# Performance work log

Measured on AMD Instinct MI355X. Metric: run time of the kernel, lower is better.

Reference implementation:

```python
import jax, jax.numpy as jnp
import numpy as np

N = 50000
DIM = 64
E = 800000


def setup_inputs() -> dict:
    key = jax.random.key(0)
    ks = jax.random.split(key, 12)
    s = 1.0 / np.sqrt(DIM)
    inp = {
        "x": jax.random.normal(ks[0], (N, DIM), dtype=jnp.float32),
        "coord": jax.random.normal(ks[1], (N, DIM), dtype=jnp.float32),
        "Wq": jax.random.uniform(ks[2], (DIM, DIM), jnp.float32, -s, s),
        "bq": jax.random.uniform(ks[3], (DIM,), jnp.float32, -s, s),
        "Wk": jax.random.uniform(ks[4], (DIM, DIM), jnp.float32, -s, s),
        "bk": jax.random.uniform(ks[5], (DIM,), jnp.float32, -s, s),
        "Wv": jax.random.uniform(ks[6], (DIM, DIM), jnp.float32, -s, s),
        "bv": jax.random.uniform(ks[7], (DIM,), jnp.float32, -s, s),
        "Wc": jax.random.uniform(ks[8], (DIM, 1), jnp.float32, -1.0, 1.0),
        "bc": jax.random.uniform(ks[9], (DIM,), jnp.float32, -1.0, 1.0),
        "edge_index": jax.random.randint(ks[10], (2, E), 0, N, dtype=jnp.int64),
    }
    return inp


def reference(x, coord, Wq, bq, Wk, bk, Wv, bv, Wc, bc, edge_index):
    row, col = edge_index[0], edge_index[1]
    # per-edge coordinate differences and distances: [E, DIM], [E, 1]
    dx = coord[row] - coord[col]
    dist = jnp.linalg.norm(dx, axis=-1, keepdims=True)
    # per-edge QKV projections (torch Linear: x @ W.T + b): [E, DIM]
    q = x[row] @ Wq.T + bq
    k = x[col] @ Wk.T + bk
    v = x[col] @ Wv.T + bv
    # scalar attention logit per edge, GLOBAL softmax over all edges (dim=0)
    attn = jnp.sum(q * k, axis=-1, keepdims=True)  # [E, 1]
    weight = jax.nn.softmax(attn, axis=0)          # [E, 1]
    delta_x = weight * v                            # [E, DIM]
    delta_coord = weight * (dist @ Wc.T + bc) * dx  # [E, DIM]
    # scatter-add back to nodes
    x_out = jax.ops.segment_sum(delta_x, row, num_segments=x.shape[0])
    coord_out = jax.ops.segment_sum(delta_coord, row, num_segments=coord.shape[0])
    return (x + x_out, coord + coord_out)
```

## Files before the change

### kernel.cpp

```cpp
#include <hip/hip_runtime.h>
#include <math.h>

#define N_NODES 50000
#define DIM 64
#define NE 800000
#define NSCAN_BLOCKS ((N_NODES + 255) / 256)

static __device__ __forceinline__ float bf2f(unsigned short u) {
    return __uint_as_float(((unsigned int)u) << 16);
}
static __device__ __forceinline__ unsigned short f2bf(float f) {
    unsigned int u = __float_as_uint(f);
    u += 0x7fffu + ((u >> 16) & 1u);
    return (unsigned short)(u >> 16);
}


__global__ __launch_bounds__(256, 5) void k_qkv(
    const float* __restrict__ x, const float* __restrict__ coord,
    const float* __restrict__ Wq, const float* __restrict__ bq,
    const float* __restrict__ Wk, const float* __restrict__ bk,
    const float* __restrict__ Wv, const float* __restrict__ bv,
    float* __restrict__ Qf, unsigned short* __restrict__ Kb,
    unsigned short* __restrict__ Vb, unsigned short* __restrict__ Cb)
{
    __shared__ ushort4 WT2[3][1024];
    __shared__ float4  xs4[32][16];

    const int tid  = threadIdx.x;
    const int base = blockIdx.x * 32;

    for (int t = tid; t < 1024; t += 256) {
        int d = t & 63, j2 = t >> 6;
        float4 a = ((const float4*)Wq)[d * 16 + j2];
        float4 b = ((const float4*)Wk)[d * 16 + j2];
        float4 c = ((const float4*)Wv)[d * 16 + j2];
        WT2[0][t] = make_ushort4(f2bf(a.x), f2bf(a.y), f2bf(a.z), f2bf(a.w));
        WT2[1][t] = make_ushort4(f2bf(b.x), f2bf(b.y), f2bf(b.z), f2bf(b.w));
        WT2[2][t] = make_ushort4(f2bf(c.x), f2bf(c.y), f2bf(c.z), f2bf(c.w));
    }
    for (int t = tid; t < 32 * DIM; t += 256) {
        if (base + (t >> 6) < N_NODES)
            Cb[(size_t)base * DIM + t] = f2bf(coord[(size_t)base * DIM + t]);
    }
    for (int t = tid; t < 512; t += 256) {
        int r = t >> 4, j2 = t & 15;
        if (base + r < N_NODES)
            xs4[r][j2] = ((const float4*)x)[(size_t)(base + r) * 16 + j2];
    }
    __syncthreads();

    const int wv = tid >> 6;
    const int d  = tid & 63;
    const float bqv = bq[d], bkv = bk[d], bvv = bv[d];

    float aq[8], ak[8], av[8];
    #pragma unroll
    for (int r = 0; r < 8; ++r) { aq[r] = bqv; ak[r] = bkv; av[r] = bvv; }

    #pragma unroll 4
    for (int j2 = 0; j2 < 16; ++j2) {
        ushort4 uq = WT2[0][j2 * 64 + d];
        ushort4 uk = WT2[1][j2 * 64 + d];
        ushort4 uv = WT2[2][j2 * 64 + d];
        float wqx = bf2f(uq.x), wqy = bf2f(uq.y), wqz = bf2f(uq.z), wqw = bf2f(uq.w);
        float wkx = bf2f(uk.x), wky = bf2f(uk.y), wkz = bf2f(uk.z), wkw = bf2f(uk.w);
        float wvx = bf2f(uv.x), wvy = bf2f(uv.y), wvz = bf2f(uv.z), wvw = bf2f(uv.w);
        #pragma unroll
        for (int r = 0; r < 8; ++r) {
            float4 xv = xs4[wv * 8 + r][j2];
            aq[r] += xv.x * wqx + xv.y * wqy + xv.z * wqz + xv.w * wqw;
            ak[r] += xv.x * wkx + xv.y * wky + xv.z * wkz + xv.w * wkw;
            av[r] += xv.x * wvx + xv.y * wvy + xv.z * wvz + xv.w * wvw;
        }
    }
    #pragma unroll
    for (int r = 0; r < 8; ++r) {
        int n = base + wv * 8 + r;
        if (n < N_NODES) {
            Qf[(size_t)n * DIM + d] = aq[r];
            Kb[(size_t)n * DIM + d] = f2bf(ak[r]);
            Vb[(size_t)n * DIM + d] = f2bf(av[r]);
        }
    }
}

__global__ __launch_bounds__(256) void k_hist(
    const int* __restrict__ eidx, int* __restrict__ counts)
{
    int e = blockIdx.x * 256 + threadIdx.x;
    if (e < NE) atomicAdd(counts + eidx[e], 1);
}

__global__ __launch_bounds__(256) void k_scan1(
    const int* __restrict__ counts, int* __restrict__ offsets,
    int* __restrict__ bsums)
{
    __shared__ int tmp[256];
    int i = blockIdx.x * 256 + threadIdx.x;
    int v = (i < N_NODES) ? counts[i] : 0;
    tmp[threadIdx.x] = v;
    __syncthreads();
    #pragma unroll
    for (int off = 1; off < 256; off <<= 1) {
        int t = (threadIdx.x >= off) ? tmp[threadIdx.x - off] : 0;
        __syncthreads();
        tmp[threadIdx.x] += t;
        __syncthreads();
    }
    if (i < N_NODES) offsets[i] = tmp[threadIdx.x] - v;
    if (threadIdx.x == 255) bsums[blockIdx.x] = tmp[255];
}

__global__ __launch_bounds__(256) void k_scan2(int* __restrict__ bsums)
{
    __shared__ int tmp[256];
    int i = threadIdx.x;
    int v = (i < NSCAN_BLOCKS) ? bsums[i] : 0;
    tmp[i] = v;
    __syncthreads();
    #pragma unroll
    for (int off = 1; off < 256; off <<= 1) {
        int t = (i >= off) ? tmp[i - off] : 0;
        __syncthreads();
        tmp[i] += t;
        __syncthreads();
    }
    if (i < NSCAN_BLOCKS) bsums[i] = tmp[i] - v;
}

__global__ __launch_bounds__(256) void k_scan3(
    int* __restrict__ offsets, int* __restrict__ counts,
    const int* __restrict__ bsums)
{
    int i = blockIdx.x * 256 + threadIdx.x;
    if (i < N_NODES) {
        int o = offsets[i] + bsums[i >> 8];
        offsets[i] = o;
        counts[i]  = o;
    }
    if (i == 0) offsets[N_NODES] = NE;
}

__global__ __launch_bounds__(256) void k_fill(
    const int* __restrict__ eidx, int* __restrict__ cursor,
    int* __restrict__ bucket_col)
{
    int e = blockIdx.x * 256 + threadIdx.x;
    if (e < NE) {
        int pos = atomicAdd(cursor + eidx[e], 1);
        bucket_col[pos] = eidx[NE + e];
    }
}

__global__ __launch_bounds__(256) void k_edge_fused(
    const int* __restrict__ bucket_col, const int* __restrict__ offsets,
    const float* __restrict__ Qf, const unsigned short* __restrict__ Kb,
    const unsigned short* __restrict__ Vb, const unsigned short* __restrict__ Cb,
    const float* __restrict__ coord,
    const float* __restrict__ Wc, const float* __restrict__ bc,
    float* __restrict__ out_x, float* __restrict__ out_c,
    float* __restrict__ wsum)
{
    const int lane = threadIdx.x & 63;
    const int n = (blockIdx.x * 256 + threadIdx.x) >> 6;
    if (n >= N_NODES) return;
    const int qt = lane >> 4;
    const int sl = lane & 15;

    const float4 q4  = ((const float4*)Qf)[(size_t)n * 16 + sl];
    const float4 cr4 = ((const float4*)coord)[(size_t)n * 16 + sl];
    const float4 wc4 = ((const float4*)Wc)[sl];
    const float4 bc4 = ((const float4*)bc)[sl];

    const int s = offsets[n], t = offsets[n + 1];
    float4 accx = {0.f, 0.f, 0.f, 0.f};
    float4 accc = {0.f, 0.f, 0.f, 0.f};
    float psum = 0.0f;

    for (int base = s; base < t; base += 8) {
        int pos0 = base + qt;
        int pos1 = base + 4 + qt;
        bool valid0 = pos0 < t, valid1 = pos1 < t;
        int pc0 = valid0 ? pos0 : (t - 1);
        int pc1 = valid1 ? pos1 : (t - 1);
        int c0 = bucket_col[pc0];
        int c1 = bucket_col[pc1];
        size_t rb0 = (size_t)c0 * 16 + sl;
        size_t rb1 = (size_t)c1 * 16 + sl;
        ushort4 ku0 = ((const ushort4*)Kb)[rb0];
        ushort4 vu0 = ((const ushort4*)Vb)[rb0];
        ushort4 cu0 = ((const ushort4*)Cb)[rb0];
        ushort4 ku1 = ((const ushort4*)Kb)[rb1];
        ushort4 vu1 = ((const ushort4*)Vb)[rb1];
        ushort4 cu1 = ((const ushort4*)Cb)[rb1];

        float d0 = q4.x * bf2f(ku0.x) + q4.y * bf2f(ku0.y)
                 + q4.z * bf2f(ku0.z) + q4.w * bf2f(ku0.w);
        float dx0x = cr4.x - bf2f(cu0.x), dx0y = cr4.y - bf2f(cu0.y);
        float dx0z = cr4.z - bf2f(cu0.z), dx0w = cr4.w - bf2f(cu0.w);
        float e0 = dx0x * dx0x + dx0y * dx0y + dx0z * dx0z + dx0w * dx0w;
        float d1 = q4.x * bf2f(ku1.x) + q4.y * bf2f(ku1.y)
                 + q4.z * bf2f(ku1.z) + q4.w * bf2f(ku1.w);
        float dx1x = cr4.x - bf2f(cu1.x), dx1y = cr4.y - bf2f(cu1.y);
        float dx1z = cr4.z - bf2f(cu1.z), dx1w = cr4.w - bf2f(cu1.w);
        float e1 = dx1x * dx1x + dx1y * dx1y + dx1z * dx1z + dx1w * dx1w;

        #pragma unroll
        for (int off = 1; off <= 8; off <<= 1) {
            d0 += __shfl_xor(d0, off);
            e0 += __shfl_xor(e0, off);
            d1 += __shfl_xor(d1, off);
            e1 += __shfl_xor(e1, off);
        }
        float p0 = valid0 ? __expf(d0) : 0.0f;
        float p1 = valid1 ? __expf(d1) : 0.0f;
        float dist0 = sqrtf(e0), dist1 = sqrtf(e1);
        psum += p0 + p1;
        accx.x += p0 * bf2f(vu0.x) + p1 * bf2f(vu1.x);
        accx.y += p0 * bf2f(vu0.y) + p1 * bf2f(vu1.y);
        accx.z += p0 * bf2f(vu0.z) + p1 * bf2f(vu1.z);
        accx.w += p0 * bf2f(vu0.w) + p1 * bf2f(vu1.w);
        accc.x += p0 * (dist0 * wc4.x + bc4.x) * dx0x
                + p1 * (dist1 * wc4.x + bc4.x) * dx1x;
        accc.y += p0 * (dist0 * wc4.y + bc4.y) * dx0y
                + p1 * (dist1 * wc4.y + bc4.y) * dx1y;
        accc.z += p0 * (dist0 * wc4.z + bc4.z) * dx0z
                + p1 * (dist1 * wc4.z + bc4.z) * dx1z;
        accc.w += p0 * (dist0 * wc4.w + bc4.w) * dx0w
                + p1 * (dist1 * wc4.w + bc4.w) * dx1w;
    }

    #pragma unroll
    for (int off = 16; off <= 32; off <<= 1) {
        accx.x += __shfl_xor(accx.x, off);
        accx.y += __shfl_xor(accx.y, off);
        accx.z += __shfl_xor(accx.z, off);
        accx.w += __shfl_xor(accx.w, off);
        accc.x += __shfl_xor(accc.x, off);
        accc.y += __shfl_xor(accc.y, off);
        accc.z += __shfl_xor(accc.z, off);
        accc.w += __shfl_xor(accc.w, off);
        psum   += __shfl_xor(psum, off);
    }
    if (lane < 16) {
        ((float4*)out_x)[(size_t)n * 16 + sl] = accx;
        ((float4*)out_c)[(size_t)n * 16 + sl] = accc;
    }
    if (lane == 0) wsum[n] = psum;
}

__global__ __launch_bounds__(1024) void k_redsum(
    const float* __restrict__ wsum, float* __restrict__ S)
{
    __shared__ float red[16];
    float a = 0.0f;
    for (int i = threadIdx.x; i < N_NODES; i += 1024) a += wsum[i];
    #pragma unroll
    for (int off = 32; off; off >>= 1) a += __shfl_xor(a, off);
    if ((threadIdx.x & 63) == 0) red[threadIdx.x >> 6] = a;
    __syncthreads();
    if (threadIdx.x == 0) {
        float s = 0.0f;
        #pragma unroll
        for (int w = 0; w < 16; ++w) s += red[w];
        *S = s;
    }
}

__global__ __launch_bounds__(256) void k_finalize(
    const float* __restrict__ x, const float* __restrict__ coord,
    const float* __restrict__ S, float* __restrict__ out)
{
    const float inv = 1.0f / *S;
    const int nd4 = (N_NODES * DIM) / 4;
    const float4* x4 = (const float4*)x;
    const float4* c4 = (const float4*)coord;
    float4* o4 = (float4*)out;
    for (int i = blockIdx.x * 256 + threadIdx.x; i < 2 * nd4;
         i += gridDim.x * 256) {
        float4 r = (i < nd4) ? x4[i] : c4[i - nd4];
        float4 a = o4[i];
        a.x = r.x + a.x * inv;
        a.y = r.y + a.y * inv;
        a.z = r.z + a.z * inv;
        a.w = r.w + a.w * inv;
        o4[i] = a;
    }
}

extern "C" void kernel_launch(void* const* d_in, const int* in_sizes, int n_in,
                              void* d_out, int out_size, void* d_ws, size_t ws_size,
                              hipStream_t stream)
{
    const float* x     = (const float*)d_in[0];
    const float* coord = (const float*)d_in[1];
    const float* Wq    = (const float*)d_in[2];
    const float* bq    = (const float*)d_in[3];
    const float* Wk    = (const float*)d_in[4];
    const float* bk    = (const float*)d_in[5];
    const float* Wv    = (const float*)d_in[6];
    const float* bv    = (const float*)d_in[7];
    const float* Wc    = (const float*)d_in[8];
    const float* bc    = (const float*)d_in[9];
    const int*   eidx  = (const int*)d_in[10];

    float* out = (float*)d_out;
    float* ws  = (float*)d_ws;

    float* Qf = ws;
    unsigned short* Kb = (unsigned short*)(Qf + (size_t)N_NODES * DIM);
    unsigned short* Vb = Kb + (size_t)N_NODES * DIM;
    unsigned short* Cb = Vb + (size_t)N_NODES * DIM;
    int* bucket_col = (int*)(Cb + (size_t)N_NODES * DIM);
    int* counts  = bucket_col + NE;
    int* offsets = counts + N_NODES;
    int* bsums   = offsets + N_NODES + 1;
    float* wsum  = (float*)(bsums + 256);
    float* S     = wsum + N_NODES;

    float* out_x = out;
    float* out_c = out + (size_t)N_NODES * DIM;

    hipMemsetAsync(counts, 0, (size_t)N_NODES * sizeof(int), stream);
    k_hist <<<(NE + 255) / 256, 256, 0, stream>>>(eidx, counts);
    k_scan1<<<NSCAN_BLOCKS, 256, 0, stream>>>(counts, offsets, bsums);
    k_scan2<<<1, 256, 0, stream>>>(bsums);
    k_scan3<<<NSCAN_BLOCKS, 256, 0, stream>>>(offsets, counts, bsums);
    k_fill <<<(NE + 255) / 256, 256, 0, stream>>>(eidx, counts, bucket_col);

    k_qkv<<<(N_NODES + 31) / 32, 256, 0, stream>>>(
        x, coord, Wq, bq, Wk, bk, Wv, bv, Qf, Kb, Vb, Cb);

    k_edge_fused<<<(N_NODES * 64 + 255) / 256, 256, 0, stream>>>(
        bucket_col, offsets, Qf, Kb, Vb, Cb, coord, Wc, bc,
        out_x, out_c, wsum);

    k_redsum<<<1, 1024, 0, stream>>>(wsum, S);
    k_finalize<<<2048, 256, 0, stream>>>(x, coord, S, out);
}
```

Before: 221.5 us.

## Interleave K/V/coord bf16 rows, merge scan kernels, atomically reduce softmax denominator

K, V and bf16 coord are packed into one 192-element row per node, so each gathered neighbour reads one contiguous 384-byte span instead of three separate rows. The second and third scan kernels are merged: each block sums the preceding block totals itself. The global softmax denominator is accumulated with a per-node atomicAdd into S, which is zeroed in the histogram kernel, removing the wsum buffer and the single-block reduction kernel. This cuts two launches but adds 50k float atomics to one address and makes the float summation order nondeterministic.

```diff
diff --git a/kernel.cpp b/kernel.cpp
--- a/kernel.cpp
+++ b/kernel.cpp
@@ -21,8 +21,7 @@
     const float* __restrict__ Wq, const float* __restrict__ bq,
     const float* __restrict__ Wk, const float* __restrict__ bk,
     const float* __restrict__ Wv, const float* __restrict__ bv,
-    float* __restrict__ Qf, unsigned short* __restrict__ Kb,
-    unsigned short* __restrict__ Vb, unsigned short* __restrict__ Cb)
+    float* __restrict__ Qf, unsigned short* __restrict__ KVCb)
 {
     __shared__ ushort4 WT2[3][1024];
     __shared__ float4  xs4[32][16];
@@ -40,8 +39,10 @@
         WT2[2][t] = make_ushort4(f2bf(c.x), f2bf(c.y), f2bf(c.z), f2bf(c.w));
     }
     for (int t = tid; t < 32 * DIM; t += 256) {
-        if (base + (t >> 6) < N_NODES)
-            Cb[(size_t)base * DIM + t] = f2bf(coord[(size_t)base * DIM + t]);
+        int gn = base + (t >> 6);
+        if (gn < N_NODES)
+            KVCb[(size_t)gn * 192 + 128 + (t & 63)] =
+                f2bf(coord[(size_t)gn * DIM + (t & 63)]);
     }
     for (int t = tid; t < 512; t += 256) {
         int r = t >> 4, j2 = t & 15;
@@ -79,17 +80,19 @@
         int n = base + wv * 8 + r;
         if (n < N_NODES) {
             Qf[(size_t)n * DIM + d] = aq[r];
-            Kb[(size_t)n * DIM + d] = f2bf(ak[r]);
-            Vb[(size_t)n * DIM + d] = f2bf(av[r]);
+            KVCb[(size_t)n * 192 + d]      = f2bf(ak[r]);
+            KVCb[(size_t)n * 192 + 64 + d] = f2bf(av[r]);
         }
     }
 }
 
 __global__ __launch_bounds__(256) void k_hist(
-    const int* __restrict__ eidx, int* __restrict__ counts)
+    const int* __restrict__ eidx, int* __restrict__ counts,
+    float* __restrict__ S)
 {
     int e = blockIdx.x * 256 + threadIdx.x;
     if (e < NE) atomicAdd(counts + eidx[e], 1);
+    if (e == 0) *S = 0.0f;
 }
 
 __global__ __launch_bounds__(256) void k_scan1(
@@ -112,30 +115,23 @@
     if (threadIdx.x == 255) bsums[blockIdx.x] = tmp[255];
 }
 
-__global__ __launch_bounds__(256) void k_scan2(int* __restrict__ bsums)
-{
-    __shared__ int tmp[256];
-    int i = threadIdx.x;
-    int v = (i < NSCAN_BLOCKS) ? bsums[i] : 0;
-    tmp[i] = v;
-    __syncthreads();
-    #pragma unroll
-    for (int off = 1; off < 256; off <<= 1) {
-        int t = (i >= off) ? tmp[i - off] : 0;
-        __syncthreads();
-        tmp[i] += t;
-        __syncthreads();
-    }
-    if (i < NSCAN_BLOCKS) bsums[i] = tmp[i] - v;
-}
-
-__global__ __launch_bounds__(256) void k_scan3(
+__global__ __launch_bounds__(256) void k_scan23(
     int* __restrict__ offsets, int* __restrict__ counts,
     const int* __restrict__ bsums)
 {
-    int i = blockIdx.x * 256 + threadIdx.x;
+    __shared__ int red[4];
+    const int tid = threadIdx.x;
+    const int b   = blockIdx.x;
+    int v = (tid < b && tid < NSCAN_BLOCKS) ? bsums[tid] : 0;
+    #pragma unroll
+    for (int off = 32; off; off >>= 1) v += __shfl_xor(v, off);
+    if ((tid & 63) == 0) red[tid >> 6] = v;
+    __syncthreads();
+    const int pre = red[0] + red[1] + red[2] + red[3];
+
+    int i = b * 256 + tid;
     if (i < N_NODES) {
-        int o = offsets[i] + bsums[i >> 8];
+        int o = offsets[i] + pre;
         offsets[i] = o;
         counts[i]  = o;
     }
@@ -155,12 +151,11 @@
 
 __global__ __launch_bounds__(256) void k_edge_fused(
     const int* __restrict__ bucket_col, const int* __restrict__ offsets,
-    const float* __restrict__ Qf, const unsigned short* __restrict__ Kb,
-    const unsigned short* __restrict__ Vb, const unsigned short* __restrict__ Cb,
+    const float* __restrict__ Qf, const unsigned short* __restrict__ KVC,
     const float* __restrict__ coord,
     const float* __restrict__ Wc, const float* __restrict__ bc,
     float* __restrict__ out_x, float* __restrict__ out_c,
-    float* __restrict__ wsum)
+    float* __restrict__ S)
 {
     const int lane = threadIdx.x & 63;
     const int n = (blockIdx.x * 256 + threadIdx.x) >> 6;
@@ -172,6 +167,7 @@
     const float4 cr4 = ((const float4*)coord)[(size_t)n * 16 + sl];
     const float4 wc4 = ((const float4*)Wc)[sl];
     const float4 bc4 = ((const float4*)bc)[sl];
+    const ushort4* KVC4 = (const ushort4*)KVC;
 
     const int s = offsets[n], t = offsets[n + 1];
     float4 accx = {0.f, 0.f, 0.f, 0.f};
@@ -184,16 +180,10 @@
         bool valid0 = pos0 < t, valid1 = pos1 < t;
         int pc0 = valid0 ? pos0 : (t - 1);
         int pc1 = valid1 ? pos1 : (t - 1);
-        int c0 = bucket_col[pc0];
-        int c1 = bucket_col[pc1];
-        size_t rb0 = (size_t)c0 * 16 + sl;
-        size_t rb1 = (size_t)c1 * 16 + sl;
-        ushort4 ku0 = ((const ushort4*)Kb)[rb0];
-        ushort4 vu0 = ((const ushort4*)Vb)[rb0];
-        ushort4 cu0 = ((const ushort4*)Cb)[rb0];
-        ushort4 ku1 = ((const ushort4*)Kb)[rb1];
-        ushort4 vu1 = ((const ushort4*)Vb)[rb1];
-        ushort4 cu1 = ((const ushort4*)Cb)[rb1];
+        const ushort4* p0 = KVC4 + (size_t)bucket_col[pc0] * 48;
+        const ushort4* p1 = KVC4 + (size_t)bucket_col[pc1] * 48;
+        ushort4 ku0 = p0[sl], vu0 = p0[sl + 16], cu0 = p0[sl + 32];
+        ushort4 ku1 = p1[sl], vu1 = p1[sl + 16], cu1 = p1[sl + 32];
 
         float d0 = q4.x * bf2f(ku0.x) + q4.y * bf2f(ku0.y)
                  + q4.z * bf2f(ku0.z) + q4.w * bf2f(ku0.w);
@@ -213,22 +203,22 @@
             d1 += __shfl_xor(d1, off);
             e1 += __shfl_xor(e1, off);
         }
-        float p0 = valid0 ? __expf(d0) : 0.0f;
-        float p1 = valid1 ? __expf(d1) : 0.0f;
+        float p0e = valid0 ? __expf(d0) : 0.0f;
+        float p1e = valid1 ? __expf(d1) : 0.0f;
         float dist0 = sqrtf(e0), dist1 = sqrtf(e1);
-        psum += p0 + p1;
-        accx.x += p0 * bf2f(vu0.x) + p1 * bf2f(vu1.x);
-        accx.y += p0 * bf2f(vu0.y) + p1 * bf2f(vu1.y);
-        accx.z += p0 * bf2f(vu0.z) + p1 * bf2f(vu1.z);
-        accx.w += p0 * bf2f(vu0.w) + p1 * bf2f(vu1.w);
-        accc.x += p0 * (dist0 * wc4.x + bc4.x) * dx0x
-                + p1 * (dist1 * wc4.x + bc4.x) * dx1x;
-        accc.y += p0 * (dist0 * wc4.y + bc4.y) * dx0y
-                + p1 * (dist1 * wc4.y + bc4.y) * dx1y;
-        accc.z += p0 * (dist0 * wc4.z + bc4.z) * dx0z
-                + p1 * (dist1 * wc4.z + bc4.z) * dx1z;
-        accc.w += p0 * (dist0 * wc4.w + bc4.w) * dx0w
-                + p1 * (dist1 * wc4.w + bc4.w) * dx1w;
+        psum += p0e + p1e;
+        accx.x += p0e * bf2f(vu0.x) + p1e * bf2f(vu1.x);
+        accx.y += p0e * bf2f(vu0.y) + p1e * bf2f(vu1.y);
+        accx.z += p0e * bf2f(vu0.z) + p1e * bf2f(vu1.z);
+        accx.w += p0e * bf2f(vu0.w) + p1e * bf2f(vu1.w);
+        accc.x += p0e * (dist0 * wc4.x + bc4.x) * dx0x
+                + p1e * (dist1 * wc4.x + bc4.x) * dx1x;
+        accc.y += p0e * (dist0 * wc4.y + bc4.y) * dx0y
+                + p1e * (dist1 * wc4.y + bc4.y) * dx1y;
+        accc.z += p0e * (dist0 * wc4.z + bc4.z) * dx0z
+                + p1e * (dist1 * wc4.z + bc4.z) * dx1z;
+        accc.w += p0e * (dist0 * wc4.w + bc4.w) * dx0w
+                + p1e * (dist1 * wc4.w + bc4.w) * dx1w;
     }
 
     #pragma unroll
@@ -247,25 +237,7 @@
         ((float4*)out_x)[(size_t)n * 16 + sl] = accx;
         ((float4*)out_c)[(size_t)n * 16 + sl] = accc;
     }
-    if (lane == 0) wsum[n] = psum;
-}
-
-__global__ __launch_bounds__(1024) void k_redsum(
-    const float* __restrict__ wsum, float* __restrict__ S)
-{
-    __shared__ float red[16];
-    float a = 0.0f;
-    for (int i = threadIdx.x; i < N_NODES; i += 1024) a += wsum[i];
-    #pragma unroll
-    for (int off = 32; off; off >>= 1) a += __shfl_xor(a, off);
-    if ((threadIdx.x & 63) == 0) red[threadIdx.x >> 6] = a;
-    __syncthreads();
-    if (threadIdx.x == 0) {
-        float s = 0.0f;
-        #pragma unroll
-        for (int w = 0; w < 16; ++w) s += red[w];
-        *S = s;
-    }
+    if (lane == 0) atomicAdd(S, psum);
 }
 
 __global__ __launch_bounds__(256) void k_finalize(
@@ -309,33 +281,27 @@
     float* ws  = (float*)d_ws;
 
     float* Qf = ws;
-    unsigned short* Kb = (unsigned short*)(Qf + (size_t)N_NODES * DIM);
-    unsigned short* Vb = Kb + (size_t)N_NODES * DIM;
-    unsigned short* Cb = Vb + (size_t)N_NODES * DIM;
-    int* bucket_col = (int*)(Cb + (size_t)N_NODES * DIM);
+    unsigned short* KVCb = (unsigned short*)(Qf + (size_t)N_NODES * DIM);
+    int* bucket_col = (int*)(KVCb + (size_t)N_NODES * 192);
     int* counts  = bucket_col + NE;
     int* offsets = counts + N_NODES;
     int* bsums   = offsets + N_NODES + 1;
-    float* wsum  = (float*)(bsums + 256);
-    float* S     = wsum + N_NODES;
+    float* S     = (float*)(bsums + 256);
 
     float* out_x = out;
     float* out_c = out + (size_t)N_NODES * DIM;
 
     hipMemsetAsync(counts, 0, (size_t)N_NODES * sizeof(int), stream);
-    k_hist <<<(NE + 255) / 256, 256, 0, stream>>>(eidx, counts);
-    k_scan1<<<NSCAN_BLOCKS, 256, 0, stream>>>(counts, offsets, bsums);
-    k_scan2<<<1, 256, 0, stream>>>(bsums);
-    k_scan3<<<NSCAN_BLOCKS, 256, 0, stream>>>(offsets, counts, bsums);
-    k_fill <<<(NE + 255) / 256, 256, 0, stream>>>(eidx, counts, bucket_col);
+    k_hist  <<<(NE + 255) / 256, 256, 0, stream>>>(eidx, counts, S);
+    k_scan1 <<<NSCAN_BLOCKS, 256, 0, stream>>>(counts, offsets, bsums);
+    k_scan23<<<NSCAN_BLOCKS, 256, 0, stream>>>(offsets, counts, bsums);
+    k_fill  <<<(NE + 255) / 256, 256, 0, stream>>>(eidx, counts, bucket_col);
 
     k_qkv<<<(N_NODES + 31) / 32, 256, 0, stream>>>(
-        x, coord, Wq, bq, Wk, bk, Wv, bv, Qf, Kb, Vb, Cb);
+        x, coord, Wq, bq, Wk, bk, Wv, bv, Qf, KVCb);
 
     k_edge_fused<<<(N_NODES * 64 + 255) / 256, 256, 0, stream>>>(
-        bucket_col, offsets, Qf, Kb, Vb, Cb, coord, Wc, bc,
-        out_x, out_c, wsum);
-
-    k_redsum<<<1, 1024, 0, stream>>>(wsum, S);
+        bucket_col, offsets, Qf, KVCb, coord, Wc, bc, out_x, out_c, S);
+
     k_finalize<<<2048, 256, 0, stream>>>(x, coord, S, out);
 }
```

After: 806.8 us. +264.2%, slower.
